# Kernel tuning notes

Hardware: AMD Instinct MI355X
Metric: run time of the kernel (lower is better)

Reference implementation:

```python
import jax, jax.numpy as jnp
import numpy as np

IN_F = 4096
OUT_F = 11008
B, S = 4, 2048

def setup_inputs() -> dict:
    key = jax.random.key(0)
    k1, k2, k3, k4 = jax.random.split(key, 4)
    x = jax.random.normal(k1, (B, S, IN_F), dtype=jnp.float16)
    # int8 quantized weights in [-127, 127]
    qweight = jax.random.randint(k2, (OUT_F, IN_F), -127, 128, dtype=jnp.int32).astype(jnp.int8)
    # per-output-channel scale: small positive values like max_abs/127
    scale = (jax.random.uniform(k3, (OUT_F,), dtype=jnp.float32) * 0.02 + 1e-4).astype(jnp.float16)
    bias = jax.random.normal(k4, (OUT_F,), dtype=jnp.float16)
    return {"x": x, "qweight": qweight, "scale": scale, "bias": bias}

def reference(x, qweight, scale, bias):
    # dequant matmul: y = (x @ W_q^T) * scale + bias, all in fp16 (act_dtype)
    x = x.astype(jnp.float16)
    w = qweight.astype(jnp.float16)          # [out, in]
    y = jnp.einsum('bsi,oi->bso', x, w)       # [B, S, out]
    y = y * scale + bias
    return y.astype(jnp.float16)
```

## Files before the change

kernel.cpp:

```cpp
#include <hip/hip_runtime.h>
#include <hip/hip_fp16.h>
#include <stdint.h>

#define M_DIM 8192
#define K_DIM 4096
#define N_DIM 11008


typedef _Float16 f16x8 __attribute__((ext_vector_type(8)));
typedef float f32x4 __attribute__((ext_vector_type(4)));

typedef const void __attribute__((address_space(1)))* gptr_t;
typedef void __attribute__((address_space(3)))* lptr_t;

__device__ __forceinline__ void async_load16(const void* g, void* l) {
    __builtin_amdgcn_global_load_lds((gptr_t)g, (lptr_t)l, 16, 0, 0);
}

__global__ void sniff_kernel(const int* __restrict__ q, int* __restrict__ flag) {
    __shared__ int s;
    if (threadIdx.x == 0) s = 1;
    __syncthreads();
    int bad = 0;
#pragma unroll
    for (int i = 0; i < 16; ++i) {
        int v = q[threadIdx.x * 16 + i];
        if (v < -127 || v > 127) bad = 1;
    }
    if (bad) s = 0;
    __syncthreads();
    if (threadIdx.x == 0) flag[0] = s;
}

__global__ __launch_bounds__(256)
void cvt_x_kernel(const float* __restrict__ in, _Float16* __restrict__ out) {
    const size_t n8 = (size_t)M_DIM * K_DIM / 8;
    const size_t stride = (size_t)gridDim.x * 256;
    for (size_t i = (size_t)blockIdx.x * 256 + threadIdx.x; i < n8; i += stride) {
        const float4* p = (const float4*)(in + i * 8);
        float4 a = p[0], b = p[1];
        f16x8 h;
        h[0] = (_Float16)a.x; h[1] = (_Float16)a.y;
        h[2] = (_Float16)a.z; h[3] = (_Float16)a.w;
        h[4] = (_Float16)b.x; h[5] = (_Float16)b.y;
        h[6] = (_Float16)b.z; h[7] = (_Float16)b.w;
        *(f16x8*)(out + i * 8) = h;
    }
}

__global__ __launch_bounds__(256)
void cvt_w_kernel(const void* __restrict__ in, _Float16* __restrict__ out,
                  const int* __restrict__ flag) {
    const bool w_is_i32 = (flag[0] != 0);
    const size_t n8 = (size_t)N_DIM * K_DIM / 8;
    const size_t stride = (size_t)gridDim.x * 256;
    if (w_is_i32) {
        const int* q = (const int*)in;
        for (size_t i = (size_t)blockIdx.x * 256 + threadIdx.x; i < n8; i += stride) {
            const int4* p = (const int4*)(q + i * 8);
            int4 a = p[0], b = p[1];
            f16x8 h;
            h[0] = (_Float16)a.x; h[1] = (_Float16)a.y;
            h[2] = (_Float16)a.z; h[3] = (_Float16)a.w;
            h[4] = (_Float16)b.x; h[5] = (_Float16)b.y;
            h[6] = (_Float16)b.z; h[7] = (_Float16)b.w;
            *(f16x8*)(out + i * 8) = h;
        }
    } else {
        const signed char* q = (const signed char*)in;
        for (size_t i = (size_t)blockIdx.x * 256 + threadIdx.x; i < n8; i += stride) {
            const int2* p = (const int2*)(q + i * 8);
            int2 raw = p[0];
            f16x8 h;
            h[0] = (_Float16)(signed char)(raw.x & 0xff);
            h[1] = (_Float16)(signed char)((raw.x >> 8) & 0xff);
            h[2] = (_Float16)(signed char)((raw.x >> 16) & 0xff);
            h[3] = (_Float16)(signed char)((raw.x >> 24) & 0xff);
            h[4] = (_Float16)(signed char)(raw.y & 0xff);
            h[5] = (_Float16)(signed char)((raw.y >> 8) & 0xff);
            h[6] = (_Float16)(signed char)((raw.y >> 16) & 0xff);
            h[7] = (_Float16)(signed char)((raw.y >> 24) & 0xff);
            *(f16x8*)(out + i * 8) = h;
        }
    }
}

#define BM 128
#define BN 128
#define FBK 64
#define TM (M_DIM / BM)
#define TN (N_DIM / BN)
#define NWG (TM * TN)
#define PER_XCD (NWG / 8)

__global__ __launch_bounds__(256)
void f16_gemm_kernel(const _Float16* __restrict__ A,
                     const _Float16* __restrict__ W,
                     const float* __restrict__ scale,
                     const float* __restrict__ bias,
                     float* __restrict__ C)
{
    __shared__ __align__(16) _Float16 As[BM * FBK];
    __shared__ __align__(16) _Float16 Bs[BN * FBK];

    const int tid  = threadIdx.x;
    const int wave = tid >> 6;
    const int lane = tid & 63;
    const int quad = lane >> 4;
    const int col  = lane & 15;

    const int bid = blockIdx.x;
    const int xcd = bid & 7;
    const int r   = bid >> 3;
    const int bm  = xcd * 8 + (r & 7);
    const int bn  = r >> 3;

    const int m0 = bm * BM;
    const int n0 = bn * BN;
    const int wm = (wave >> 1) * 64;
    const int wn = (wave & 1) * 64;

    f32x4 acc[4][4];
#pragma unroll
    for (int mi = 0; mi < 4; ++mi)
#pragma unroll
        for (int ni = 0; ni < 4; ++ni)
            acc[mi][ni] = (f32x4){0.f, 0.f, 0.f, 0.f};

    const int srow   = tid >> 3;
    const int schunk = (tid & 7) ^ (srow & 7);
    const _Float16* ga = A + (size_t)(m0 + srow) * K_DIM + schunk * 8;
    const _Float16* gw = W + (size_t)(n0 + srow) * K_DIM + schunk * 8;
    _Float16* la = As + tid * 8;
    _Float16* lb = Bs + tid * 8;

    for (int k0 = 0; k0 < K_DIM; k0 += FBK) {
#pragma unroll
        for (int i = 0; i < 4; ++i) {
            async_load16(ga + (size_t)i * 32 * K_DIM + k0, la + i * 2048);
            async_load16(gw + (size_t)i * 32 * K_DIM + k0, lb + i * 2048);
        }
        __syncthreads();

#pragma unroll
        for (int ks = 0; ks < 2; ++ks) {
            const int cx = ((ks * 4 + quad) ^ (col & 7)) * 8;
            f16x8 af[4], bf[4];
#pragma unroll
            for (int mi = 0; mi < 4; ++mi)
                af[mi] = *(const f16x8*)(As + (wm + mi * 16 + col) * FBK + cx);
#pragma unroll
            for (int ni = 0; ni < 4; ++ni)
                bf[ni] = *(const f16x8*)(Bs + (wn + ni * 16 + col) * FBK + cx);
#pragma unroll
            for (int mi = 0; mi < 4; ++mi)
#pragma unroll
                for (int ni = 0; ni < 4; ++ni)
                    acc[mi][ni] = __builtin_amdgcn_mfma_f32_16x16x32_f16(
                        af[mi], bf[ni], acc[mi][ni], 0, 0, 0);
        }
        __syncthreads();
    }

    float scl[4], bsv[4];
#pragma unroll
    for (int ni = 0; ni < 4; ++ni) {
        int n = n0 + wn + ni * 16 + col;
        scl[ni] = scale[n];
        bsv[ni] = bias[n];
    }
#pragma unroll
    for (int mi = 0; mi < 4; ++mi) {
#pragma unroll
        for (int rr = 0; rr < 4; ++rr) {
            int m = m0 + wm + mi * 16 + quad * 4 + rr;
            float* cp = C + (size_t)m * N_DIM + n0 + wn + col;
#pragma unroll
            for (int ni = 0; ni < 4; ++ni) {
                cp[ni * 16] = acc[mi][ni][rr] * scl[ni] + bsv[ni];
            }
        }
    }
}

#define OBK 32

__global__ __launch_bounds__(256)
void w8_gemm_kernel(const float* __restrict__ A,
                    const void* __restrict__ Wv,
                    const float* __restrict__ scale,
                    const float* __restrict__ bias,
                    float* __restrict__ C,
                    const int* __restrict__ flag)
{
    __shared__ __align__(16) _Float16 As[BM * OBK];
    __shared__ __align__(16) _Float16 Bs[BN * OBK];

    const int tid  = threadIdx.x;
    const int wave = tid >> 6;
    const int lane = tid & 63;
    const int quad = lane >> 4;
    const int col  = lane & 15;

    const bool w_is_i32 = (flag[0] != 0);

    int bid = blockIdx.x;
    const int per_group = 8 * TN;
    int g = bid / per_group;
    int r = bid - g * per_group;
    const int bm = g * 8 + (r & 7);
    const int bn = r >> 3;

    const int m0 = bm * BM;
    const int n0 = bn * BN;
    const int wm = (wave >> 1) * 64;
    const int wn = (wave & 1) * 64;

    f32x4 acc[4][4];
#pragma unroll
    for (int mi = 0; mi < 4; ++mi)
#pragma unroll
        for (int ni = 0; ni < 4; ++ni)
            acc[mi][ni] = (f32x4){0.f, 0.f, 0.f, 0.f};

    for (int k0 = 0; k0 < K_DIM; k0 += OBK) {
#pragma unroll
        for (int i = 0; i < 2; ++i) {
            int idx = i * 256 + tid;
            int row = idx >> 2;
            int c   = idx & 3;
            const float4* p = (const float4*)(A + (size_t)(m0 + row) * K_DIM + k0 + c * 8);
            float4 v0 = p[0];
            float4 v1 = p[1];
            f16x8 h;
            h[0] = (_Float16)v0.x; h[1] = (_Float16)v0.y;
            h[2] = (_Float16)v0.z; h[3] = (_Float16)v0.w;
            h[4] = (_Float16)v1.x; h[5] = (_Float16)v1.y;
            h[6] = (_Float16)v1.z; h[7] = (_Float16)v1.w;
            *(f16x8*)(As + idx * 8) = h;
        }
        if (w_is_i32) {
            const int* Wq = (const int*)Wv;
#pragma unroll
            for (int i = 0; i < 2; ++i) {
                int idx = i * 256 + tid;
                int row = idx >> 2;
                int c   = idx & 3;
                const int4* p = (const int4*)(Wq + (size_t)(n0 + row) * K_DIM + k0 + c * 8);
                int4 a = p[0];
                int4 b = p[1];
                f16x8 h;
                h[0] = (_Float16)a.x; h[1] = (_Float16)a.y;
                h[2] = (_Float16)a.z; h[3] = (_Float16)a.w;
                h[4] = (_Float16)b.x; h[5] = (_Float16)b.y;
                h[6] = (_Float16)b.z; h[7] = (_Float16)b.w;
                *(f16x8*)(Bs + idx * 8) = h;
            }
        } else {
            const signed char* W8 = (const signed char*)Wv;
#pragma unroll
            for (int i = 0; i < 2; ++i) {
                int idx = i * 256 + tid;
                int row = idx >> 2;
                int c   = idx & 3;
                const int2* p = (const int2*)(W8 + (size_t)(n0 + row) * K_DIM + k0 + c * 8);
                int2 raw = p[0];
                f16x8 h;
                h[0] = (_Float16)(signed char)(raw.x & 0xff);
                h[1] = (_Float16)(signed char)((raw.x >> 8) & 0xff);
                h[2] = (_Float16)(signed char)((raw.x >> 16) & 0xff);
                h[3] = (_Float16)(signed char)((raw.x >> 24) & 0xff);
                h[4] = (_Float16)(signed char)(raw.y & 0xff);
                h[5] = (_Float16)(signed char)((raw.y >> 8) & 0xff);
                h[6] = (_Float16)(signed char)((raw.y >> 16) & 0xff);
                h[7] = (_Float16)(signed char)((raw.y >> 24) & 0xff);
                *(f16x8*)(Bs + idx * 8) = h;
            }
        }
        __syncthreads();

        f16x8 af[4], bfr[4];
#pragma unroll
        for (int mi = 0; mi < 4; ++mi)
            af[mi] = *(const f16x8*)(As + (wm + mi * 16 + col) * OBK + quad * 8);
#pragma unroll
        for (int ni = 0; ni < 4; ++ni)
            bfr[ni] = *(const f16x8*)(Bs + (wn + ni * 16 + col) * OBK + quad * 8);
#pragma unroll
        for (int mi = 0; mi < 4; ++mi)
#pragma unroll
            for (int ni = 0; ni < 4; ++ni)
                acc[mi][ni] = __builtin_amdgcn_mfma_f32_16x16x32_f16(
                    af[mi], bfr[ni], acc[mi][ni], 0, 0, 0);
        __syncthreads();
    }

    float scl[4], bs[4];
#pragma unroll
    for (int ni = 0; ni < 4; ++ni) {
        int n = n0 + wn + ni * 16 + col;
        scl[ni] = scale[n];
        bs[ni]  = bias[n];
    }
#pragma unroll
    for (int mi = 0; mi < 4; ++mi) {
#pragma unroll
        for (int rr = 0; rr < 4; ++rr) {
            int m = m0 + wm + mi * 16 + quad * 4 + rr;
            float* cp = C + (size_t)m * N_DIM + n0 + wn + col;
#pragma unroll
            for (int ni = 0; ni < 4; ++ni) {
                cp[ni * 16] = acc[mi][ni][rr] * scl[ni] + bs[ni];
            }
        }
    }
}

extern "C" void kernel_launch(void* const* d_in, const int* in_sizes, int n_in,
                              void* d_out, int out_size, void* d_ws, size_t ws_size,
                              hipStream_t stream) {
    const float* x     = (const float*)d_in[0];
    const void*  qw    = d_in[1];
    const float* scale = (const float*)d_in[2];
    const float* bias  = (const float*)d_in[3];
    float* out = (float*)d_out;

    int* flag = (int*)d_ws;

    const size_t A_BYTES = (size_t)M_DIM * K_DIM * 2;
    const size_t W_BYTES = (size_t)N_DIM * K_DIM * 2;
    const size_t NEED    = 256 + A_BYTES + W_BYTES;

    sniff_kernel<<<1, 256, 0, stream>>>((const int*)qw, flag);

    if (ws_size >= NEED) {
        _Float16* Ah = (_Float16*)((char*)d_ws + 256);
        _Float16* Wh = (_Float16*)((char*)d_ws + 256 + A_BYTES);
        cvt_x_kernel<<<2048, 256, 0, stream>>>(x, Ah);
        cvt_w_kernel<<<2048, 256, 0, stream>>>(qw, Wh, flag);
        f16_gemm_kernel<<<NWG, 256, 0, stream>>>(Ah, Wh, scale, bias, out);
    } else {
        w8_gemm_kernel<<<TM * TN, 256, 0, stream>>>(x, qw, scale, bias, out, flag);
    }
}
```

Before: 1.437 ms.

## Use 256x256 double-buffered fp16 GEMM tile with 8 waves and MFMA priority

Replaces the 128x128 single-buffered fp16 GEMM with a 256x256 tile run by 512 threads. Each wave now computes a 128x64 sub-tile, which raises arithmetic intensity per LDS and global byte. K tiles are double-buffered in LDS so the next tile's async loads overlap the current tile's MFMAs, with one barrier per iteration. s_setprio is raised around the MFMA blocks. The trade-off is 128KB of LDS and many more accumulator registers per block, which limits occupancy to about one block per CU.

```diff
diff --git a/kernel.cpp b/kernel.cpp
--- a/kernel.cpp
+++ b/kernel.cpp
@@ -15,6 +15,13 @@
 
 __device__ __forceinline__ void async_load16(const void* g, void* l) {
     __builtin_amdgcn_global_load_lds((gptr_t)g, (lptr_t)l, 16, 0, 0);
+}
+
+__device__ __forceinline__ void tile_barrier() {
+    __builtin_amdgcn_sched_barrier(0);
+    asm volatile("s_waitcnt vmcnt(0)" ::: "memory");
+    __builtin_amdgcn_s_barrier();
+    __builtin_amdgcn_sched_barrier(0);
 }
 
 __global__ void sniff_kernel(const int* __restrict__ q, int* __restrict__ flag) {
@@ -85,23 +92,22 @@
     }
 }
 
-#define BM 128
-#define BN 128
-#define FBK 64
-#define TM (M_DIM / BM)
-#define TN (N_DIM / BN)
-#define NWG (TM * TN)
-#define PER_XCD (NWG / 8)
-
-__global__ __launch_bounds__(256)
-void f16_gemm_kernel(const _Float16* __restrict__ A,
-                     const _Float16* __restrict__ W,
-                     const float* __restrict__ scale,
-                     const float* __restrict__ bias,
-                     float* __restrict__ C)
+#define BM2 256
+#define BN2 256
+#define BK2 64
+#define TM2 (M_DIM / BM2)
+#define TN2 (N_DIM / BN2)
+#define NWG2 (TM2 * TN2)
+
+__global__ __launch_bounds__(512, 2)
+void f16_gemm256_kernel(const _Float16* __restrict__ A,
+                        const _Float16* __restrict__ W,
+                        const float* __restrict__ scale,
+                        const float* __restrict__ bias,
+                        float* __restrict__ C)
 {
-    __shared__ __align__(16) _Float16 As[BM * FBK];
-    __shared__ __align__(16) _Float16 Bs[BN * FBK];
+    __shared__ __align__(16) _Float16 As[2 * BM2 * BK2];
+    __shared__ __align__(16) _Float16 Bs[2 * BN2 * BK2];
 
     const int tid  = threadIdx.x;
     const int wave = tid >> 6;
@@ -112,54 +118,129 @@
     const int bid = blockIdx.x;
     const int xcd = bid & 7;
     const int r   = bid >> 3;
-    const int bm  = xcd * 8 + (r & 7);
-    const int bn  = r >> 3;
-
-    const int m0 = bm * BM;
-    const int n0 = bn * BN;
-    const int wm = (wave >> 1) * 64;
-    const int wn = (wave & 1) * 64;
-
-    f32x4 acc[4][4];
-#pragma unroll
-    for (int mi = 0; mi < 4; ++mi)
-#pragma unroll
-        for (int ni = 0; ni < 4; ++ni)
-            acc[mi][ni] = (f32x4){0.f, 0.f, 0.f, 0.f};
+    const int bm  = xcd * 4 + r / TN2;
+    const int bn  = r % TN2;
+
+    const int m0 = bm * BM2;
+    const int n0 = bn * BN2;
+    const int wm = (wave >> 2) * 128;
+    const int wn = (wave & 3) * 64;
+
+    f32x4 acc[8][4];
+#pragma unroll
+    for (int i = 0; i < 8; ++i)
+#pragma unroll
+        for (int j = 0; j < 4; ++j)
+            acc[i][j] = (f32x4){0.f, 0.f, 0.f, 0.f};
 
     const int srow   = tid >> 3;
     const int schunk = (tid & 7) ^ (srow & 7);
     const _Float16* ga = A + (size_t)(m0 + srow) * K_DIM + schunk * 8;
     const _Float16* gw = W + (size_t)(n0 + srow) * K_DIM + schunk * 8;
-    _Float16* la = As + tid * 8;
-    _Float16* lb = Bs + tid * 8;
-
-    for (int k0 = 0; k0 < K_DIM; k0 += FBK) {
-#pragma unroll
-        for (int i = 0; i < 4; ++i) {
-            async_load16(ga + (size_t)i * 32 * K_DIM + k0, la + i * 2048);
-            async_load16(gw + (size_t)i * 32 * K_DIM + k0, lb + i * 2048);
-        }
-        __syncthreads();
-
-#pragma unroll
-        for (int ks = 0; ks < 2; ++ks) {
-            const int cx = ((ks * 4 + quad) ^ (col & 7)) * 8;
-            f16x8 af[4], bf[4];
-#pragma unroll
-            for (int mi = 0; mi < 4; ++mi)
-                af[mi] = *(const f16x8*)(As + (wm + mi * 16 + col) * FBK + cx);
-#pragma unroll
-            for (int ni = 0; ni < 4; ++ni)
-                bf[ni] = *(const f16x8*)(Bs + (wn + ni * 16 + col) * FBK + cx);
-#pragma unroll
-            for (int mi = 0; mi < 4; ++mi)
-#pragma unroll
-                for (int ni = 0; ni < 4; ++ni)
-                    acc[mi][ni] = __builtin_amdgcn_mfma_f32_16x16x32_f16(
-                        af[mi], bf[ni], acc[mi][ni], 0, 0, 0);
-        }
-        __syncthreads();
+
+    const int cx0 = ((0 * 4 + quad) ^ (col & 7)) * 8;
+    const int cx1 = ((1 * 4 + quad) ^ (col & 7)) * 8;
+
+#pragma unroll
+    for (int i = 0; i < 4; ++i) {
+        async_load16(ga + (size_t)i * 64 * K_DIM, As + tid * 8 + i * 4096);
+        async_load16(gw + (size_t)i * 64 * K_DIM, Bs + tid * 8 + i * 4096);
+    }
+    tile_barrier();
+
+    const int NT = K_DIM / BK2;
+#pragma unroll 2
+    for (int t = 0; t < NT; ++t) {
+        const int cur = t & 1;
+        const _Float16* Ab = As + cur * (BM2 * BK2);
+        const _Float16* Bb = Bs + cur * (BN2 * BK2);
+
+        if (t + 1 < NT) {
+            const int nxt = cur ^ 1;
+            const int k1 = (t + 1) * BK2;
+            _Float16* la = As + nxt * (BM2 * BK2) + tid * 8;
+            _Float16* lb = Bs + nxt * (BN2 * BK2) + tid * 8;
+#pragma unroll
+            for (int i = 0; i < 4; ++i) {
+                async_load16(ga + (size_t)i * 64 * K_DIM + k1, la + i * 4096);
+                async_load16(gw + (size_t)i * 64 * K_DIM + k1, lb + i * 4096);
+            }
+        }
+
+        f16x8 a[8], bq[8];
+#pragma unroll
+        for (int mi = 0; mi < 4; ++mi) {
+            const _Float16* ap = Ab + (wm + mi * 16 + col) * BK2;
+            a[mi * 2 + 0] = *(const f16x8*)(ap + cx0);
+            a[mi * 2 + 1] = *(const f16x8*)(ap + cx1);
+        }
+#pragma unroll
+        for (int ni = 0; ni < 2; ++ni) {
+            const _Float16* bp = Bb + (wn + ni * 16 + col) * BK2;
+            bq[ni * 2 + 0] = *(const f16x8*)(bp + cx0);
+            bq[ni * 2 + 1] = *(const f16x8*)(bp + cx1);
+        }
+        __builtin_amdgcn_s_setprio(1);
+#pragma unroll
+        for (int mi = 0; mi < 4; ++mi)
+#pragma unroll
+            for (int ni = 0; ni < 2; ++ni) {
+                acc[mi][ni] = __builtin_amdgcn_mfma_f32_16x16x32_f16(
+                    a[mi * 2 + 0], bq[ni * 2 + 0], acc[mi][ni], 0, 0, 0);
+                acc[mi][ni] = __builtin_amdgcn_mfma_f32_16x16x32_f16(
+                    a[mi * 2 + 1], bq[ni * 2 + 1], acc[mi][ni], 0, 0, 0);
+            }
+        __builtin_amdgcn_s_setprio(0);
+
+#pragma unroll
+        for (int ni = 2; ni < 4; ++ni) {
+            const _Float16* bp = Bb + (wn + ni * 16 + col) * BK2;
+            bq[ni * 2 + 0] = *(const f16x8*)(bp + cx0);
+            bq[ni * 2 + 1] = *(const f16x8*)(bp + cx1);
+        }
+        __builtin_amdgcn_s_setprio(1);
+#pragma unroll
+        for (int mi = 0; mi < 4; ++mi)
+#pragma unroll
+            for (int ni = 2; ni < 4; ++ni) {
+                acc[mi][ni] = __builtin_amdgcn_mfma_f32_16x16x32_f16(
+                    a[mi * 2 + 0], bq[ni * 2 + 0], acc[mi][ni], 0, 0, 0);
+                acc[mi][ni] = __builtin_amdgcn_mfma_f32_16x16x32_f16(
+                    a[mi * 2 + 1], bq[ni * 2 + 1], acc[mi][ni], 0, 0, 0);
+            }
+        __builtin_amdgcn_s_setprio(0);
+
+#pragma unroll
+        for (int mi = 0; mi < 4; ++mi) {
+            const _Float16* ap = Ab + (wm + 64 + mi * 16 + col) * BK2;
+            a[mi * 2 + 0] = *(const f16x8*)(ap + cx0);
+            a[mi * 2 + 1] = *(const f16x8*)(ap + cx1);
+        }
+        __builtin_amdgcn_s_setprio(1);
+#pragma unroll
+        for (int mi = 0; mi < 4; ++mi)
+#pragma unroll
+            for (int ni = 0; ni < 2; ++ni) {
+                acc[4 + mi][ni] = __builtin_amdgcn_mfma_f32_16x16x32_f16(
+                    a[mi * 2 + 0], bq[ni * 2 + 0], acc[4 + mi][ni], 0, 0, 0);
+                acc[4 + mi][ni] = __builtin_amdgcn_mfma_f32_16x16x32_f16(
+                    a[mi * 2 + 1], bq[ni * 2 + 1], acc[4 + mi][ni], 0, 0, 0);
+            }
+        __builtin_amdgcn_s_setprio(0);
+
+        __builtin_amdgcn_s_setprio(1);
+#pragma unroll
+        for (int mi = 0; mi < 4; ++mi)
+#pragma unroll
+            for (int ni = 2; ni < 4; ++ni) {
+                acc[4 + mi][ni] = __builtin_amdgcn_mfma_f32_16x16x32_f16(
+                    a[mi * 2 + 0], bq[ni * 2 + 0], acc[4 + mi][ni], 0, 0, 0);
+                acc[4 + mi][ni] = __builtin_amdgcn_mfma_f32_16x16x32_f16(
+                    a[mi * 2 + 1], bq[ni * 2 + 1], acc[4 + mi][ni], 0, 0, 0);
+            }
+        __builtin_amdgcn_s_setprio(0);
+
+        tile_barrier();
     }
 
     float scl[4], bsv[4];
@@ -170,20 +251,27 @@
         bsv[ni] = bias[n];
     }
 #pragma unroll
-    for (int mi = 0; mi < 4; ++mi) {
-#pragma unroll
-        for (int rr = 0; rr < 4; ++rr) {
-            int m = m0 + wm + mi * 16 + quad * 4 + rr;
-            float* cp = C + (size_t)m * N_DIM + n0 + wn + col;
-#pragma unroll
-            for (int ni = 0; ni < 4; ++ni) {
-                cp[ni * 16] = acc[mi][ni][rr] * scl[ni] + bsv[ni];
-            }
-        }
-    }
-}
-
+    for (int rh = 0; rh < 2; ++rh) {
+#pragma unroll
+        for (int mi = 0; mi < 4; ++mi) {
+#pragma unroll
+            for (int rr = 0; rr < 4; ++rr) {
+                int m = m0 + wm + rh * 64 + mi * 16 + quad * 4 + rr;
+                float* cp = C + (size_t)m * N_DIM + n0 + wn + col;
+#pragma unroll
+                for (int ni = 0; ni < 4; ++ni) {
+                    cp[ni * 16] = acc[rh * 4 + mi][ni][rr] * scl[ni] + bsv[ni];
+                }
+            }
+        }
+    }
+}
+
+#define BM 128
+#define BN 128
 #define OBK 32
+#define TM (M_DIM / BM)
+#define TN (N_DIM / BN)
 
 __global__ __launch_bounds__(256)
 void w8_gemm_kernel(const float* __restrict__ A,
@@ -338,7 +426,7 @@
         _Float16* Wh = (_Float16*)((char*)d_ws + 256 + A_BYTES);
         cvt_x_kernel<<<2048, 256, 0, stream>>>(x, Ah);
         cvt_w_kernel<<<2048, 256, 0, stream>>>(qw, Wh, flag);
-        f16_gemm_kernel<<<NWG, 256, 0, stream>>>(Ah, Wh, scale, bias, out);
+        f16_gemm256_kernel<<<NWG2, 512, 0, stream>>>(Ah, Wh, scale, bias, out);
     } else {
         w8_gemm_kernel<<<TM * TN, 256, 0, stream>>>(x, qw, scale, bias, out, flag);
     }
```

New measurement: 1.261 ms. -12.3%, faster.
